# Kernel tuning notes

Measured on AMD Instinct MI355X. Metric: run time of the kernel, lower is better.

Reference implementation:

```python
import jax, jax.numpy as jnp
import numpy as np

V, E, H, L, T, B = 6500, 192, 6, 6, 512, 32
HS = E // H  # 32
EPS = 1e-5


def setup_inputs() -> dict:
    key = jax.random.key(0)
    ks = jax.random.split(key, 9)
    s = 0.02
    return {
        "idx": jax.random.randint(ks[0], (B, T), 0, V, dtype=jnp.int32),
        "tok_emb": jax.random.normal(ks[1], (V, E), dtype=jnp.float32) * s,
        "Wq": jax.random.normal(ks[2], (L, E, E), dtype=jnp.float32) * s,
        "Wk": jax.random.normal(ks[3], (L, E, E), dtype=jnp.float32) * s,
        "Wv": jax.random.normal(ks[4], (L, E, E), dtype=jnp.float32) * s,
        "Wo": jax.random.normal(ks[5], (L, E, E), dtype=jnp.float32) * s,
        "W1": jax.random.normal(ks[6], (L, E, 4 * E), dtype=jnp.float32) * s,
        "W2": jax.random.normal(ks[7], (L, 4 * E, E), dtype=jnp.float32) * s,
        "ln1_g": jnp.ones((L, E)), "ln1_b": jnp.zeros((L, E)),
        "ln2_g": jnp.ones((L, E)), "ln2_b": jnp.zeros((L, E)),
        "lnf_g": jnp.ones((E,)), "lnf_b": jnp.zeros((E,)),
        "Wlm": jax.random.normal(ks[8], (E, V), dtype=jnp.float32) * s,
    }


def _layer_norm(x, g, b):
    mu = jnp.mean(x, axis=-1, keepdims=True)
    var = jnp.mean(jnp.square(x - mu), axis=-1, keepdims=True)
    return (x - mu) * jax.lax.rsqrt(var + EPS) * g + b


def _sinusoidal(t, d):
    pos = jnp.arange(t, dtype=jnp.float32)[:, None]
    div = jnp.exp(jnp.arange(0, d, 2, dtype=jnp.float32) * (-np.log(10000.0) / d))
    pe = jnp.zeros((t, d), dtype=jnp.float32)
    pe = pe.at[:, 0::2].set(jnp.sin(pos * div))
    pe = pe.at[:, 1::2].set(jnp.cos(pos * div))
    return pe


def reference(idx, tok_emb, Wq, Wk, Wv, Wo, W1, W2,
              ln1_g, ln1_b, ln2_g, ln2_b, lnf_g, lnf_b, Wlm):
    x = tok_emb[idx] + _sinusoidal(T, E)[None, :, :]  # [B,T,E]
    mask = jnp.tril(jnp.ones((T, T), dtype=bool))
    scale = E ** (-0.5)  # NOTE: original scales by n_embd**-0.5, not head_size

    def block(x, p):
        l1g, l1b, wq, wk, wv, wo, l2g, l2b, w1, w2 = p
        h = _layer_norm(x, l1g, l1b)
        q = jnp.einsum('bte,ehd->bhtd', h, wq.reshape(E, H, HS))
        k = jnp.einsum('bte,ehd->bhtd', h, wk.reshape(E, H, HS))
        v = jnp.einsum('bte,ehd->bhtd', h, wv.reshape(E, H, HS))
        wei = jnp.einsum('bhtd,bhsd->bhts', q, k) * scale  # [B,H,T,T]
        wei = jnp.where(mask, wei, -jnp.inf)
        wei = jax.nn.softmax(wei, axis=-1)
        att = jnp.einsum('bhts,bhsd->bthd', wei, v).reshape(B, T, E)
        x = x + att @ wo
        h2 = _layer_norm(x, l2g, l2b)
        x = x + jax.nn.gelu(h2 @ w1, approximate=False) @ w2
        return x, None

    x, _ = jax.lax.scan(block, x, (ln1_g, ln1_b, Wq, Wk, Wv, Wo, ln2_g, ln2_b, W1, W2))
    x = _layer_norm(x, lnf_g, lnf_b)
    return x @ Wlm  # [B,T,V] logits
```

## Files before the change

kernel.cpp:

```cpp
#include <hip/hip_runtime.h>
#include <hip/hip_bf16.h>
#include <math.h>

#define VOCAB 6500
#define EMB   192
#define NH    6
#define NL    6
#define SEQ   512
#define BATCH 32
#define HSZ   32
#define BT    (BATCH*SEQ)

typedef __attribute__((ext_vector_type(8))) short bh8;
typedef __attribute__((ext_vector_type(4))) float f32x4;

#define ATT_SCALE 0.07216878364870323f

__global__ __launch_bounds__(256) void embed_ln(
    const int* __restrict__ idx, const float* __restrict__ tok,
    const float* __restrict__ g, const float* __restrict__ b,
    float* __restrict__ x, __hip_bfloat16* __restrict__ h) {
  const int wid = threadIdx.x >> 6, lane = threadIdx.x & 63;
  const int bt = blockIdx.x * 4 + wid;
  const int t  = bt & (SEQ - 1);
  const int tokid = idx[bt];
  float v[3];
  #pragma unroll
  for (int i = 0; i < 3; ++i) {
    const int e = lane + i * 64;
    const int i2 = e & ~1;
    const float div = expf((float)i2 * (-9.210340371976184f / (float)EMB));
    const float ang = (float)t * div;
    const float pe  = (e & 1) ? cosf(ang) : sinf(ang);
    v[i] = tok[(size_t)tokid * EMB + e] + pe;
  }
  float s = v[0] + v[1] + v[2];
  #pragma unroll
  for (int o = 32; o; o >>= 1) s += __shfl_xor(s, o);
  const float mu = s * (1.0f / (float)EMB);
  float vs = 0.f;
  #pragma unroll
  for (int i = 0; i < 3; ++i) { const float d = v[i] - mu; vs += d * d; }
  #pragma unroll
  for (int o = 32; o; o >>= 1) vs += __shfl_xor(vs, o);
  const float r = rsqrtf(vs * (1.0f / (float)EMB) + 1e-5f);
  float* xr = x + (size_t)bt * EMB;
  __hip_bfloat16* hr = h + (size_t)bt * EMB;
  #pragma unroll
  for (int i = 0; i < 3; ++i) {
    const int e = lane + i * 64;
    xr[e] = v[i];
    hr[e] = __float2bfloat16((v[i] - mu) * r * g[e] + b[e]);
  }
}

__global__ __launch_bounds__(256) void wcast(
    const float* __restrict__ W, __hip_bfloat16* __restrict__ Wt,
    int K, int N, int dstride) {
  __shared__ float t[32][33];
  const float* Ws = W + (size_t)blockIdx.z * K * N;
  __hip_bfloat16* Wd = Wt + (size_t)blockIdx.z * dstride * K;
  const int kt = blockIdx.y * 32, nt = blockIdx.x * 32;
  const int tx = threadIdx.x, ty = threadIdx.y;
  for (int i = ty; i < 32; i += 8) {
    const int k = kt + i, n = nt + tx;
    t[i][tx] = (k < K && n < N) ? Ws[(size_t)k * N + n] : 0.f;
  }
  __syncthreads();
  for (int i = ty; i < 32; i += 8) {
    const int n = nt + i, k = kt + tx;
    if (n < N && k < K) Wd[(size_t)n * K + k] = __float2bfloat16(t[tx][i]);
  }
}

__global__ __launch_bounds__(256) void wcast4(
    const float* __restrict__ Wq, const float* __restrict__ Wk,
    const float* __restrict__ Wv, const float* __restrict__ Wo,
    __hip_bfloat16* __restrict__ wqkv, __hip_bfloat16* __restrict__ wot) {
  __shared__ float t[32][33];
  const int z = blockIdx.z, sel = z / NL, layer = z % NL;
  const float* srcs[4] = {Wq, Wk, Wv, Wo};
  const float* Ws = srcs[sel] + (size_t)layer * EMB * EMB;
  __hip_bfloat16* Wd = (sel < 3)
      ? wqkv + ((size_t)layer * 576 + sel * 192) * EMB
      : wot  + (size_t)layer * EMB * EMB;
  const int kt = blockIdx.y * 32, nt = blockIdx.x * 32;
  const int tx = threadIdx.x, ty = threadIdx.y;
  for (int i = ty; i < 32; i += 8)
    t[i][tx] = Ws[(size_t)(kt + i) * EMB + nt + tx];
  __syncthreads();
  for (int i = ty; i < 32; i += 8)
    Wd[(size_t)(nt + i) * EMB + kt + tx] = __float2bfloat16(t[tx][i]);
}

template<int EPI, int BN>
__global__ __launch_bounds__(256) void gemm_big(
    const __hip_bfloat16* __restrict__ A, const __hip_bfloat16* __restrict__ Bt,
    void* __restrict__ Cv, int M, int N, int K) {
  constexpr int LDK = 72;
  constexpr int NB = BN / 32;
  constexpr int NC = BN / 16;
  __shared__ short As[128 * LDK];
  __shared__ short Bs[BN * LDK];
  const int tid = threadIdx.x;
  const int wid = tid >> 6, lane = tid & 63;
  const int m0 = blockIdx.y * 128, n0 = blockIdx.x * BN;
  const int srow = tid >> 3, schk = tid & 7;
  const int fr = lane & 15, fg = lane >> 4;

  f32x4 acc[2][NC];
  #pragma unroll
  for (int rt = 0; rt < 2; ++rt)
    #pragma unroll
    for (int ct = 0; ct < NC; ++ct) acc[rt][ct] = (f32x4){0.f, 0.f, 0.f, 0.f};

  bh8 av[4], bv[NB];
  #pragma unroll
  for (int p = 0; p < 4; ++p)
    av[p] = *reinterpret_cast<const bh8*>(A + (size_t)(m0 + srow + p * 32) * K + schk * 8);
  #pragma unroll
  for (int p = 0; p < NB; ++p) {
    const int nr = n0 + srow + p * 32;
    if (nr < N) bv[p] = *reinterpret_cast<const bh8*>(Bt + (size_t)nr * K + schk * 8);
    else        bv[p] = (bh8){0,0,0,0,0,0,0,0};
  }

  for (int k0 = 0; k0 < K; k0 += 64) {
    __syncthreads();
    #pragma unroll
    for (int p = 0; p < 4; ++p)
      *reinterpret_cast<bh8*>(As + (srow + p * 32) * LDK + schk * 8) = av[p];
    #pragma unroll
    for (int p = 0; p < NB; ++p)
      *reinterpret_cast<bh8*>(Bs + (srow + p * 32) * LDK + schk * 8) = bv[p];
    __syncthreads();
    if (k0 + 64 < K) {
      const int kn = k0 + 64 + schk * 8;
      #pragma unroll
      for (int p = 0; p < 4; ++p)
        av[p] = *reinterpret_cast<const bh8*>(A + (size_t)(m0 + srow + p * 32) * K + kn);
      #pragma unroll
      for (int p = 0; p < NB; ++p) {
        const int nr = n0 + srow + p * 32;
        if (nr < N) bv[p] = *reinterpret_cast<const bh8*>(Bt + (size_t)nr * K + kn);
      }
    }
    #pragma unroll
    for (int s = 0; s < 2; ++s) {
      bh8 af[2];
      #pragma unroll
      for (int rt = 0; rt < 2; ++rt)
        af[rt] = *reinterpret_cast<const bh8*>(As + (wid * 32 + rt * 16 + fr) * LDK + s * 32 + fg * 8);
      #pragma unroll
      for (int ct = 0; ct < NC; ++ct) {
        const bh8 bf_ = *reinterpret_cast<const bh8*>(Bs + (ct * 16 + fr) * LDK + s * 32 + fg * 8);
        #pragma unroll
        for (int rt = 0; rt < 2; ++rt)
          acc[rt][ct] = __builtin_amdgcn_mfma_f32_16x16x32_bf16(af[rt], bf_, acc[rt][ct], 0, 0, 0);
      }
    }
  }

  #pragma unroll
  for (int rt = 0; rt < 2; ++rt)
    #pragma unroll
    for (int ct = 0; ct < NC; ++ct) {
      const int col = n0 + ct * 16 + fr;
      if (col < N) {
        #pragma unroll
        for (int rr = 0; rr < 4; ++rr) {
          const int row = m0 + wid * 32 + rt * 16 + fg * 4 + rr;
          float v = acc[rt][ct][rr];
          if (EPI == 0) {
            ((float*)Cv)[(size_t)row * N + col] = v;
          } else if (EPI == 2) {
            v = 0.5f * v * (1.0f + erff(v * 0.70710678118654752f));
            ((__hip_bfloat16*)Cv)[(size_t)row * N + col] = __float2bfloat16(v);
          } else {
            const int part = col / 192, c2 = col - part * 192;
            if (part == 0) v *= ATT_SCALE;
            const int bb = row >> 9, tt = row & (SEQ - 1);
            const int hh = c2 >> 5, dd = c2 & (HSZ - 1);
            ((__hip_bfloat16*)Cv)[(size_t)part * BT * EMB +
                (((size_t)(bb * NH + hh)) * SEQ + tt) * HSZ + dd] = __float2bfloat16(v);
          }
        }
      }
    }
}

__global__ __launch_bounds__(128) void gemm_resln(
    const __hip_bfloat16* __restrict__ A, const __hip_bfloat16* __restrict__ Bt,
    float* __restrict__ X, __hip_bfloat16* __restrict__ Hout,
    const float* __restrict__ g, const float* __restrict__ b, int K) {
  constexpr int LDK = 72;
  __shared__ short As[32 * LDK];
  __shared__ short Bs[192 * LDK];
  const int tid = threadIdx.x;
  const int wid = tid >> 6, lane = tid & 63;
  const int m0 = blockIdx.x * 32;
  const int srow = tid >> 3, schk = tid & 7;
  const int fr = lane & 15, fg = lane >> 4;

  f32x4 acc[12];
  #pragma unroll
  for (int j = 0; j < 12; ++j) acc[j] = (f32x4){0.f, 0.f, 0.f, 0.f};

  bh8 av[2], bv[12];
  #pragma unroll
  for (int p = 0; p < 2; ++p)
    av[p] = *reinterpret_cast<const bh8*>(A + (size_t)(m0 + srow + p * 16) * K + schk * 8);
  #pragma unroll
  for (int p = 0; p < 12; ++p)
    bv[p] = *reinterpret_cast<const bh8*>(Bt + (size_t)(srow + p * 16) * K + schk * 8);

  for (int k0 = 0; k0 < K; k0 += 64) {
    __syncthreads();
    #pragma unroll
    for (int p = 0; p < 2; ++p)
      *reinterpret_cast<bh8*>(As + (srow + p * 16) * LDK + schk * 8) = av[p];
    #pragma unroll
    for (int p = 0; p < 12; ++p)
      *reinterpret_cast<bh8*>(Bs + (srow + p * 16) * LDK + schk * 8) = bv[p];
    __syncthreads();
    if (k0 + 64 < K) {
      const int kn = k0 + 64 + schk * 8;
      #pragma unroll
      for (int p = 0; p < 2; ++p)
        av[p] = *reinterpret_cast<const bh8*>(A + (size_t)(m0 + srow + p * 16) * K + kn);
      #pragma unroll
      for (int p = 0; p < 12; ++p)
        bv[p] = *reinterpret_cast<const bh8*>(Bt + (size_t)(srow + p * 16) * K + kn);
    }
    #pragma unroll
    for (int s = 0; s < 2; ++s) {
      const bh8 af = *reinterpret_cast<const bh8*>(As + (wid * 16 + fr) * LDK + s * 32 + fg * 8);
      #pragma unroll
      for (int j = 0; j < 12; ++j) {
        const bh8 bf_ = *reinterpret_cast<const bh8*>(Bs + (j * 16 + fr) * LDK + s * 32 + fg * 8);
        acc[j] = __builtin_amdgcn_mfma_f32_16x16x32_bf16(af, bf_, acc[j], 0, 0, 0);
      }
    }
  }

  #pragma unroll
  for (int rr = 0; rr < 4; ++rr) {
    const int row = m0 + wid * 16 + fg * 4 + rr;
    float v[12], sum = 0.f, sq = 0.f;
    #pragma unroll
    for (int j = 0; j < 12; ++j) {
      v[j] = acc[j][rr] + X[(size_t)row * EMB + j * 16 + fr];
      sum += v[j]; sq += v[j] * v[j];
    }
    #pragma unroll
    for (int o = 8; o; o >>= 1) {
      sum += __shfl_xor(sum, o);
      sq  += __shfl_xor(sq,  o);
    }
    const float mu = sum * (1.0f / (float)EMB);
    const float r  = rsqrtf(sq * (1.0f / (float)EMB) - mu * mu + 1e-5f);
    #pragma unroll
    for (int j = 0; j < 12; ++j) {
      const int col = j * 16 + fr;
      X[(size_t)row * EMB + col] = v[j];
      Hout[(size_t)row * EMB + col] = __float2bfloat16((v[j] - mu) * r * g[col] + b[col]);
    }
  }
}

__global__ __launch_bounds__(256) void flash_attn(
    const __hip_bfloat16* __restrict__ qh, const __hip_bfloat16* __restrict__ kh,
    const __hip_bfloat16* __restrict__ vh, __hip_bfloat16* __restrict__ att) {
  constexpr int QT = 128, KT = 64, LDP = 72;
  __shared__ __hip_bfloat16 Ks[KT * LDP];
  __shared__ __hip_bfloat16 Vs[HSZ * LDP];
  __shared__ __hip_bfloat16 Ps[4][32 * LDP];
  const int qt = blockIdx.x, h = blockIdx.y, b = blockIdx.z;
  const int tid = threadIdx.x, wid = tid >> 6, lane = tid & 63;
  const int q0 = qt * QT;
  const size_t hb = ((size_t)(b * NH + h)) * SEQ * HSZ;
  const int fr = lane & 15, fg = lane >> 4;

  bh8 aq[2];
  #pragma unroll
  for (int rt = 0; rt < 2; ++rt)
    aq[rt] = *reinterpret_cast<const bh8*>(
        qh + hb + (size_t)(q0 + wid * 32 + rt * 16 + fr) * HSZ + fg * 8);

  f32x4 o[2][2];
  float lp[2][4];
  #pragma unroll
  for (int rt = 0; rt < 2; ++rt) {
    #pragma unroll
    for (int ct = 0; ct < 2; ++ct) o[rt][ct] = (f32x4){0.f, 0.f, 0.f, 0.f};
    #pragma unroll
    for (int rr = 0; rr < 4; ++rr) lp[rt][rr] = 0.f;
  }

  const int nt = 2 * qt + 2;
  const int sr = tid >> 2, d0 = (tid & 3) * 8;
  bh8 kv8 = *reinterpret_cast<const bh8*>(kh + hb + (size_t)sr * HSZ + d0);
  bh8 vv8 = *reinterpret_cast<const bh8*>(vh + hb + (size_t)sr * HSZ + d0);

  for (int it = 0; it < nt; ++it) {
    const int s0 = it * KT;
    __syncthreads();
    {
      *reinterpret_cast<bh8*>(&Ks[sr * LDP + d0]) = kv8;
      short tmp[8]; *reinterpret_cast<bh8*>(tmp) = vv8;
      #pragma unroll
      for (int j = 0; j < 8; ++j)
        Vs[(d0 + j) * LDP + sr] = *reinterpret_cast<__hip_bfloat16*>(&tmp[j]);
    }
    __syncthreads();
    if (it + 1 < nt) {
      const size_t nb_ = hb + (size_t)(s0 + KT + sr) * HSZ + d0;
      kv8 = *reinterpret_cast<const bh8*>(kh + nb_);
      vv8 = *reinterpret_cast<const bh8*>(vh + nb_);
    }

    f32x4 sfr[2][4];
    #pragma unroll
    for (int rt = 0; rt < 2; ++rt)
      #pragma unroll
      for (int st = 0; st < 4; ++st) {
        const bh8 bf_ = *reinterpret_cast<const bh8*>(&Ks[(st * 16 + fr) * LDP + fg * 8]);
        sfr[rt][st] = __builtin_amdgcn_mfma_f32_16x16x32_bf16(
            aq[rt], bf_, (f32x4){0.f, 0.f, 0.f, 0.f}, 0, 0, 0);
      }

    __hip_bfloat16* Pw = Ps[wid];
    const bool diag = (s0 + KT - 1 > q0 + wid * 32);
    #pragma unroll
    for (int rt = 0; rt < 2; ++rt) {
      #pragma unroll
      for (int rr = 0; rr < 4; ++rr) {
        float pr[4];
        if (diag) {
          const int qa = q0 + wid * 32 + rt * 16 + fg * 4 + rr;
          #pragma unroll
          for (int st = 0; st < 4; ++st) {
            const int sa = s0 + st * 16 + fr;
            pr[st] = (sa > qa) ? 0.f : __expf(sfr[rt][st][rr]);
          }
        } else {
          #pragma unroll
          for (int st = 0; st < 4; ++st) pr[st] = __expf(sfr[rt][st][rr]);
        }
        lp[rt][rr] += (pr[0] + pr[1]) + (pr[2] + pr[3]);
        #pragma unroll
        for (int st = 0; st < 4; ++st)
          Pw[(rt * 16 + fg * 4 + rr) * LDP + st * 16 + fr] = __float2bfloat16(pr[st]);
      }
    }

    #pragma unroll
    for (int ks = 0; ks < 2; ++ks) {
      bh8 vb_[2];
      #pragma unroll
      for (int ct = 0; ct < 2; ++ct)
        vb_[ct] = *reinterpret_cast<const bh8*>(&Vs[(ct * 16 + fr) * LDP + ks * 32 + fg * 8]);
      #pragma unroll
      for (int rt = 0; rt < 2; ++rt) {
        const bh8 pa = *reinterpret_cast<const bh8*>(&Pw[(rt * 16 + fr) * LDP + ks * 32 + fg * 8]);
        #pragma unroll
        for (int ct = 0; ct < 2; ++ct)
          o[rt][ct] = __builtin_amdgcn_mfma_f32_16x16x32_bf16(pa, vb_[ct], o[rt][ct], 0, 0, 0);
      }
    }
  }

  #pragma unroll
  for (int rt = 0; rt < 2; ++rt)
    #pragma unroll
    for (int rr = 0; rr < 4; ++rr) {
      float s = lp[rt][rr];
      #pragma unroll
      for (int off = 8; off; off >>= 1) s += __shfl_xor(s, off);
      const float inv = 1.0f / s;
      const int qa = q0 + wid * 32 + rt * 16 + fg * 4 + rr;
      #pragma unroll
      for (int ct = 0; ct < 2; ++ct) {
        const int d = ct * 16 + fr;
        att[((size_t)(b * SEQ + qa)) * EMB + h * HSZ + d] =
            __float2bfloat16(o[rt][ct][rr] * inv);
      }
    }
}

extern "C" void kernel_launch(void* const* d_in, const int* in_sizes, int n_in,
                              void* d_out, int out_size, void* d_ws, size_t ws_size,
                              hipStream_t stream) {
  const int*   idx   = (const int*)  d_in[0];
  const float* tok   = (const float*)d_in[1];
  const float* Wq    = (const float*)d_in[2];
  const float* Wk    = (const float*)d_in[3];
  const float* Wv    = (const float*)d_in[4];
  const float* Wo    = (const float*)d_in[5];
  const float* W1    = (const float*)d_in[6];
  const float* W2    = (const float*)d_in[7];
  const float* ln1g  = (const float*)d_in[8];
  const float* ln1b  = (const float*)d_in[9];
  const float* ln2g  = (const float*)d_in[10];
  const float* ln2b  = (const float*)d_in[11];
  const float* lnfg  = (const float*)d_in[12];
  const float* lnfb  = (const float*)d_in[13];
  const float* Wlm   = (const float*)d_in[14];
  float* out = (float*)d_out;

  const size_t NTE = (size_t)BT * EMB;
  char* ws = (char*)d_ws;
  float* x   = (float*)ws;                         ws += NTE * 4;
  __hip_bfloat16* qh   = (__hip_bfloat16*)ws;      ws += NTE * 2 * 3;
  __hip_bfloat16* h    = (__hip_bfloat16*)ws;      ws += NTE * 2;
  __hip_bfloat16* att  = (__hip_bfloat16*)ws;      ws += NTE * 2;
  __hip_bfloat16* hid  = (__hip_bfloat16*)ws;      ws += NTE * 4 * 2;
  __hip_bfloat16* wqkv = (__hip_bfloat16*)ws;      ws += (size_t)NL * 576 * EMB * 2;
  __hip_bfloat16* wot  = (__hip_bfloat16*)ws;      ws += (size_t)NL * EMB * EMB * 2;
  __hip_bfloat16* w1t  = (__hip_bfloat16*)ws;      ws += (size_t)NL * EMB * EMB * 4 * 2;
  __hip_bfloat16* w2t  = (__hip_bfloat16*)ws;      ws += (size_t)NL * EMB * EMB * 4 * 2;
  __hip_bfloat16* wlt  = (__hip_bfloat16*)ws;

  const dim3 tblk(32, 8);
  wcast4<<<dim3(6, 6, 4 * NL), tblk, 0, stream>>>(Wq, Wk, Wv, Wo, wqkv, wot);
  wcast<<<dim3(24, 6, NL),  tblk, 0, stream>>>(W1,  w1t, EMB, EMB * 4, EMB * 4);
  wcast<<<dim3(6, 24, NL),  tblk, 0, stream>>>(W2,  w2t, EMB * 4, EMB, EMB);
  wcast<<<dim3(204, 6, 1),  tblk, 0, stream>>>(Wlm, wlt, EMB, VOCAB, VOCAB);

  embed_ln<<<BT / 4, 256, 0, stream>>>(idx, tok, ln1g, ln1b, x, h);

  const dim3 gQKV(576 / 64, BT / 128);
  const dim3 gM  (EMB * 4 / 64, BT / 128);
  const dim3 gV  ((VOCAB + 127) / 128, BT / 128);
  const dim3 gA  (SEQ / 128, NH, BATCH);

  for (int l = 0; l < NL; ++l) {
    const size_t wo = (size_t)l * EMB * EMB;
    const size_t wm = (size_t)l * EMB * EMB * 4;
    gemm_big<3, 64><<<gQKV, 256, 0, stream>>>(h, wqkv + (size_t)l * 576 * EMB, qh, BT, 576, EMB);
    flash_attn<<<gA, 256, 0, stream>>>(qh, qh + NTE, qh + 2 * NTE, att);
    gemm_resln<<<BT / 32, 128, 0, stream>>>(att, wot + wo, x, h,
                                            ln2g + l * EMB, ln2b + l * EMB, EMB);
    gemm_big<2, 64><<<gM, 256, 0, stream>>>(h, w1t + wm, hid, BT, EMB * 4, EMB);
    const float* ng = (l == NL - 1) ? lnfg : ln1g + (l + 1) * EMB;
    const float* nb = (l == NL - 1) ? lnfb : ln1b + (l + 1) * EMB;
    gemm_resln<<<BT / 32, 128, 0, stream>>>(hid, w2t + wm, x, h, ng, nb, EMB * 4);
  }

  gemm_big<0, 128><<<gV, 256, 0, stream>>>(h, wlt, out, BT, VOCAB, EMB);
}
```

Baseline: 706.9 us.

## Widen attention key tiles, reverse query-tile order, and merge weight-cast kernels

The flash attention kernel now processes 128-key tiles instead of 64, halving loop iterations and barriers per query tile. It also launches the heaviest causal query tiles first to reduce tail imbalance. The four weight transpose/cast launches are merged into a single kernel to cut launch overhead. Larger tiles increase registers and LDS use per block, which may lower occupancy, and the diagonal tile now wastes more masked work.

```diff
diff --git a/kernel.cpp b/kernel.cpp
--- a/kernel.cpp
+++ b/kernel.cpp
@@ -54,14 +54,42 @@
   }
 }
 
-__global__ __launch_bounds__(256) void wcast(
-    const float* __restrict__ W, __hip_bfloat16* __restrict__ Wt,
-    int K, int N, int dstride) {
+__global__ __launch_bounds__(256) void wprep(
+    const float* __restrict__ Wq, const float* __restrict__ Wk,
+    const float* __restrict__ Wv, const float* __restrict__ Wo,
+    const float* __restrict__ W1, const float* __restrict__ W2,
+    const float* __restrict__ Wlm,
+    __hip_bfloat16* __restrict__ wqkv, __hip_bfloat16* __restrict__ wot,
+    __hip_bfloat16* __restrict__ w1t,  __hip_bfloat16* __restrict__ w2t,
+    __hip_bfloat16* __restrict__ wlt) {
   __shared__ float t[32][33];
-  const float* Ws = W + (size_t)blockIdx.z * K * N;
-  __hip_bfloat16* Wd = Wt + (size_t)blockIdx.z * dstride * K;
-  const int kt = blockIdx.y * 32, nt = blockIdx.x * 32;
-  const int tx = threadIdx.x, ty = threadIdx.y;
+  const int id = blockIdx.x;
+  const float* Ws; __hip_bfloat16* Wd; int K, N, bx, by;
+  if (id < 864) {
+    const int z = id / 36, rem = id % 36;
+    const int sel = z / NL, layer = z % NL;
+    by = rem / 6; bx = rem % 6; K = 192; N = 192;
+    const float* s4[4] = {Wq, Wk, Wv, Wo};
+    Ws = s4[sel] + (size_t)layer * 192 * 192;
+    Wd = (sel < 3) ? wqkv + ((size_t)layer * 576 + sel * 192) * 192
+                   : wot  + (size_t)layer * 192 * 192;
+  } else if (id < 1728) {
+    const int j = id - 864, layer = j / 144, rem = j % 144;
+    bx = rem % 24; by = rem / 24; K = 192; N = 768;
+    Ws = W1 + (size_t)layer * 192 * 768;
+    Wd = w1t + (size_t)layer * 768 * 192;
+  } else if (id < 2592) {
+    const int j = id - 1728, layer = j / 144, rem = j % 144;
+    bx = rem % 6; by = rem / 6; K = 768; N = 192;
+    Ws = W2 + (size_t)layer * 768 * 192;
+    Wd = w2t + (size_t)layer * 192 * 768;
+  } else {
+    const int j = id - 2592;
+    bx = j % 204; by = j / 204; K = 192; N = VOCAB;
+    Ws = Wlm; Wd = wlt;
+  }
+  const int kt = by * 32, nt = bx * 32;
+  const int tx = threadIdx.x & 31, ty = threadIdx.x >> 5;
   for (int i = ty; i < 32; i += 8) {
     const int k = kt + i, n = nt + tx;
     t[i][tx] = (k < K && n < N) ? Ws[(size_t)k * N + n] : 0.f;
@@ -71,26 +99,6 @@
     const int n = nt + i, k = kt + tx;
     if (n < N && k < K) Wd[(size_t)n * K + k] = __float2bfloat16(t[tx][i]);
   }
-}
-
-__global__ __launch_bounds__(256) void wcast4(
-    const float* __restrict__ Wq, const float* __restrict__ Wk,
-    const float* __restrict__ Wv, const float* __restrict__ Wo,
-    __hip_bfloat16* __restrict__ wqkv, __hip_bfloat16* __restrict__ wot) {
-  __shared__ float t[32][33];
-  const int z = blockIdx.z, sel = z / NL, layer = z % NL;
-  const float* srcs[4] = {Wq, Wk, Wv, Wo};
-  const float* Ws = srcs[sel] + (size_t)layer * EMB * EMB;
-  __hip_bfloat16* Wd = (sel < 3)
-      ? wqkv + ((size_t)layer * 576 + sel * 192) * EMB
-      : wot  + (size_t)layer * EMB * EMB;
-  const int kt = blockIdx.y * 32, nt = blockIdx.x * 32;
-  const int tx = threadIdx.x, ty = threadIdx.y;
-  for (int i = ty; i < 32; i += 8)
-    t[i][tx] = Ws[(size_t)(kt + i) * EMB + nt + tx];
-  __syncthreads();
-  for (int i = ty; i < 32; i += 8)
-    Wd[(size_t)(nt + i) * EMB + kt + tx] = __float2bfloat16(t[tx][i]);
 }
 
 template<int EPI, int BN>
@@ -271,11 +279,14 @@
 __global__ __launch_bounds__(256) void flash_attn(
     const __hip_bfloat16* __restrict__ qh, const __hip_bfloat16* __restrict__ kh,
     const __hip_bfloat16* __restrict__ vh, __hip_bfloat16* __restrict__ att) {
-  constexpr int QT = 128, KT = 64, LDP = 72;
-  __shared__ __hip_bfloat16 Ks[KT * LDP];
-  __shared__ __hip_bfloat16 Vs[HSZ * LDP];
-  __shared__ __hip_bfloat16 Ps[4][32 * LDP];
-  const int qt = blockIdx.x, h = blockIdx.y, b = blockIdx.z;
+  constexpr int QT = 128, KT = 128;
+  constexpr int LK = 40;
+  constexpr int LS = 136;
+  __shared__ __hip_bfloat16 Ks[KT * LK];
+  __shared__ __hip_bfloat16 Vs[HSZ * LS];
+  __shared__ __hip_bfloat16 Ps[4][32 * LS];
+  const int qt = (SEQ / QT - 1) - blockIdx.x;
+  const int h = blockIdx.y, b = blockIdx.z;
   const int tid = threadIdx.x, wid = tid >> 6, lane = tid & 63;
   const int q0 = qt * QT;
   const size_t hb = ((size_t)(b * NH + h)) * SEQ * HSZ;
@@ -297,34 +308,44 @@
     for (int rr = 0; rr < 4; ++rr) lp[rt][rr] = 0.f;
   }
 
-  const int nt = 2 * qt + 2;
-  const int sr = tid >> 2, d0 = (tid & 3) * 8;
-  bh8 kv8 = *reinterpret_cast<const bh8*>(kh + hb + (size_t)sr * HSZ + d0);
-  bh8 vv8 = *reinterpret_cast<const bh8*>(vh + hb + (size_t)sr * HSZ + d0);
+  const int nt = qt + 1;
+  const int sr = tid >> 1;
+  const int dbase = (tid & 1) * 16;
+  bh8 kv[2], vv[2];
+  #pragma unroll
+  for (int i = 0; i < 2; ++i) {
+    kv[i] = *reinterpret_cast<const bh8*>(kh + hb + (size_t)sr * HSZ + dbase + i * 8);
+    vv[i] = *reinterpret_cast<const bh8*>(vh + hb + (size_t)sr * HSZ + dbase + i * 8);
+  }
 
   for (int it = 0; it < nt; ++it) {
     const int s0 = it * KT;
     __syncthreads();
-    {
-      *reinterpret_cast<bh8*>(&Ks[sr * LDP + d0]) = kv8;
-      short tmp[8]; *reinterpret_cast<bh8*>(tmp) = vv8;
+    #pragma unroll
+    for (int i = 0; i < 2; ++i) {
+      const int d0 = dbase + i * 8;
+      *reinterpret_cast<bh8*>(&Ks[sr * LK + d0]) = kv[i];
+      short tmp[8]; *reinterpret_cast<bh8*>(tmp) = vv[i];
       #pragma unroll
       for (int j = 0; j < 8; ++j)
-        Vs[(d0 + j) * LDP + sr] = *reinterpret_cast<__hip_bfloat16*>(&tmp[j]);
+        Vs[(d0 + j) * LS + sr] = *reinterpret_cast<__hip_bfloat16*>(&tmp[j]);
     }
     __syncthreads();
     if (it + 1 < nt) {
-      const size_t nb_ = hb + (size_t)(s0 + KT + sr) * HSZ + d0;
-      kv8 = *reinterpret_cast<const bh8*>(kh + nb_);
-      vv8 = *reinterpret_cast<const bh8*>(vh + nb_);
-    }
-
-    f32x4 sfr[2][4];
+      const size_t nb_ = hb + (size_t)(s0 + KT + sr) * HSZ + dbase;
+      #pragma unroll
+      for (int i = 0; i < 2; ++i) {
+        kv[i] = *reinterpret_cast<const bh8*>(kh + nb_ + i * 8);
+        vv[i] = *reinterpret_cast<const bh8*>(vh + nb_ + i * 8);
+      }
+    }
+
+    f32x4 sfr[2][8];
     #pragma unroll
     for (int rt = 0; rt < 2; ++rt)
       #pragma unroll
-      for (int st = 0; st < 4; ++st) {
-        const bh8 bf_ = *reinterpret_cast<const bh8*>(&Ks[(st * 16 + fr) * LDP + fg * 8]);
+      for (int st = 0; st < 8; ++st) {
+        const bh8 bf_ = *reinterpret_cast<const bh8*>(&Ks[(st * 16 + fr) * LK + fg * 8]);
         sfr[rt][st] = __builtin_amdgcn_mfma_f32_16x16x32_bf16(
             aq[rt], bf_, (f32x4){0.f, 0.f, 0.f, 0.f}, 0, 0, 0);
       }
@@ -335,34 +356,37 @@
     for (int rt = 0; rt < 2; ++rt) {
       #pragma unroll
       for (int rr = 0; rr < 4; ++rr) {
-        float pr[4];
+        float pr[8];
         if (diag) {
           const int qa = q0 + wid * 32 + rt * 16 + fg * 4 + rr;
           #pragma unroll
-          for (int st = 0; st < 4; ++st) {
+          for (int st = 0; st < 8; ++st) {
             const int sa = s0 + st * 16 + fr;
             pr[st] = (sa > qa) ? 0.f : __expf(sfr[rt][st][rr]);
           }
         } else {
           #pragma unroll
-          for (int st = 0; st < 4; ++st) pr[st] = __expf(sfr[rt][st][rr]);
+          for (int st = 0; st < 8; ++st) pr[st] = __expf(sfr[rt][st][rr]);
         }
-        lp[rt][rr] += (pr[0] + pr[1]) + (pr[2] + pr[3]);
+        float ls = 0.f;
         #pragma unroll
-        for (int st = 0; st < 4; ++st)
-          Pw[(rt * 16 + fg * 4 + rr) * LDP + st * 16 + fr] = __float2bfloat16(pr[st]);
-      }
-    }
-
-    #pragma unroll
-    for (int ks = 0; ks < 2; ++ks) {
+        for (int st = 0; st < 8; ++st) ls += pr[st];
+        lp[rt][rr] += ls;
+        #pragma unroll
+        for (int st = 0; st < 8; ++st)
+          Pw[(rt * 16 + fg * 4 + rr) * LS + st * 16 + fr] = __float2bfloat16(pr[st]);
+      }
+    }
+
+    #pragma unroll
+    for (int ks = 0; ks < 4; ++ks) {
       bh8 vb_[2];
       #pragma unroll
       for (int ct = 0; ct < 2; ++ct)
-        vb_[ct] = *reinterpret_cast<const bh8*>(&Vs[(ct * 16 + fr) * LDP + ks * 32 + fg * 8]);
+        vb_[ct] = *reinterpret_cast<const bh8*>(&Vs[(ct * 16 + fr) * LS + ks * 32 + fg * 8]);
       #pragma unroll
       for (int rt = 0; rt < 2; ++rt) {
-        const bh8 pa = *reinterpret_cast<const bh8*>(&Pw[(rt * 16 + fr) * LDP + ks * 32 + fg * 8]);
+        const bh8 pa = *reinterpret_cast<const bh8*>(&Pw[(rt * 16 + fr) * LS + ks * 32 + fg * 8]);
         #pragma unroll
         for (int ct = 0; ct < 2; ++ct)
           o[rt][ct] = __builtin_amdgcn_mfma_f32_16x16x32_bf16(pa, vb_[ct], o[rt][ct], 0, 0, 0);
@@ -421,12 +445,8 @@
   __hip_bfloat16* w2t  = (__hip_bfloat16*)ws;      ws += (size_t)NL * EMB * EMB * 4 * 2;
   __hip_bfloat16* wlt  = (__hip_bfloat16*)ws;
 
-  const dim3 tblk(32, 8);
-  wcast4<<<dim3(6, 6, 4 * NL), tblk, 0, stream>>>(Wq, Wk, Wv, Wo, wqkv, wot);
-  wcast<<<dim3(24, 6, NL),  tblk, 0, stream>>>(W1,  w1t, EMB, EMB * 4, EMB * 4);
-  wcast<<<dim3(6, 24, NL),  tblk, 0, stream>>>(W2,  w2t, EMB * 4, EMB, EMB);
-  wcast<<<dim3(204, 6, 1),  tblk, 0, stream>>>(Wlm, wlt, EMB, VOCAB, VOCAB);
-
+  wprep<<<3816, 256, 0, stream>>>(Wq, Wk, Wv, Wo, W1, W2, Wlm,
+                                  wqkv, wot, w1t, w2t, wlt);
   embed_ln<<<BT / 4, 256, 0, stream>>>(idx, tok, ln1g, ln1b, x, h);
 
   const dim3 gQKV(576 / 64, BT / 128);
```

New measurement: 704.8 us. No clear change (-0.3%).
